# Performance work log

Hardware: AMD Instinct MI355X
Metric: run time of the kernel (lower is better)

Reference implementation:

```python
import jax, jax.numpy as jnp
import numpy as np

IN_F = 512
OUT_F = 256
ALPHA = 0.2  # LeakyReLU negative slope
NEG_INF = -9e15


def setup_inputs() -> dict:
    key = jax.random.key(0)
    k1, k2, k3, k4 = jax.random.split(key, 4)
    N = 8192
    inp = jax.random.normal(k1, (N, IN_F), dtype=jnp.float32)
    adj = jax.random.randint(k2, (N, N), 0, 2, dtype=jnp.int32)
    # xavier_normal with gain=1.414
    std_W = 1.414 * np.sqrt(2.0 / (IN_F + OUT_F))
    W = jax.random.normal(k3, (IN_F, OUT_F), dtype=jnp.float32) * std_W
    std_a = 1.414 * np.sqrt(2.0 / (2 * OUT_F + 1))
    a = jax.random.normal(k4, (2 * OUT_F, 1), dtype=jnp.float32) * std_a
    return {"input": inp, "adj": adj, "W": W, "a": a}


def reference(input, adj, W, a):
    h = input @ W                              # [N, F]
    attn_self = h @ a[:OUT_F]                  # [N, 1]
    attn_neigh = h @ a[OUT_F:]                 # [N, 1]
    dense = attn_self + attn_neigh.T           # [N, N] broadcast add
    dense = jnp.where(dense >= 0, dense, ALPHA * dense)  # leaky relu
    scores = jnp.where(adj > 0, dense, NEG_INF)
    attention = jax.nn.softmax(scores, axis=1)  # dropout p=0.0 -> identity
    h_prime = attention @ h                     # [N, F]
    return jax.nn.elu(h_prime)                  # concat=True branch
```

## Files before the change

kernel.cpp:

```cpp
#include <hip/hip_runtime.h>
#include <hip/hip_bf16.h>
#include <math.h>

#define DEVI static __device__ __forceinline__

using f32x4  = __attribute__((ext_vector_type(4))) float;
using f32x16 = __attribute__((ext_vector_type(16))) float;
using s16x8  = __attribute__((ext_vector_type(8))) short;
using bf16x8 = __attribute__((ext_vector_type(8))) __bf16;
using i32x4  = __attribute__((ext_vector_type(4))) int;
using u32x2  = __attribute__((ext_vector_type(2))) unsigned int;
using u32x4  = __attribute__((ext_vector_type(4))) unsigned int;

constexpr int N   = 8192;
constexpr int KIN = 512;
constexpr int F   = 256;

DEVI unsigned f2bf(float f) {
  unsigned u = __builtin_bit_cast(unsigned, f);
  return ((u + 0x7FFFu + ((u >> 16) & 1u)) >> 16) & 0xFFFFu;
}

DEVI float bfLO(unsigned u) { return __builtin_bit_cast(float, (u & 0xFFFFu) << 16); }
DEVI float bfHI(unsigned u) { return __builtin_bit_cast(float, u & 0xFFFF0000u); }

DEVI unsigned cvtpk(float lo, float hi) {
  unsigned r;
  asm("v_cvt_pk_bf16_f32 %0, %1, %2" : "=v"(r) : "v"(lo), "v"(hi));
  return r;
}

DEVI f32x16 mfma32(s16x8 a, s16x8 b, f32x16 c) {
  return __builtin_amdgcn_mfma_f32_32x32x16_bf16(
      __builtin_bit_cast(bf16x8, a), __builtin_bit_cast(bf16x8, b), c, 0, 0, 0);
}

DEVI void gload16(const void* g, void* lds_uniform) {
  __builtin_amdgcn_global_load_lds(
      (const __attribute__((address_space(1))) unsigned*)g,
      (__attribute__((address_space(3))) unsigned*)lds_uniform, 16, 0, 0);
}

__global__ __launch_bounds__(256) void k_cast(const float* __restrict__ src,
                                              unsigned short* __restrict__ dst,
                                              int n8) {
  int t = blockIdx.x * 256 + threadIdx.x;
  if (t >= n8) return;
  const f32x4* p = (const f32x4*)(src + (size_t)t * 8);
  f32x4 v0 = p[0], v1 = p[1];
  s16x8 o;
  o[0] = (short)f2bf(v0[0]); o[1] = (short)f2bf(v0[1]);
  o[2] = (short)f2bf(v0[2]); o[3] = (short)f2bf(v0[3]);
  o[4] = (short)f2bf(v1[0]); o[5] = (short)f2bf(v1[1]);
  o[6] = (short)f2bf(v1[2]); o[7] = (short)f2bf(v1[3]);
  *(s16x8*)(dst + (size_t)t * 8) = o;
}

__global__ __launch_bounds__(256) void k_prep_w(const float* __restrict__ W,
                                                unsigned short* __restrict__ Wt) {
  int t = blockIdx.x * 256 + threadIdx.x;
  int c = t >> 6, k0 = (t & 63) * 8;
  s16x8 o;
#pragma unroll
  for (int i = 0; i < 8; ++i) o[i] = (short)f2bf(W[(size_t)(k0 + i) * F + c]);
  *(s16x8*)(Wt + (size_t)c * KIN + k0) = o;
}

__global__ __launch_bounds__(512) void k_gemm1(const unsigned short* __restrict__ inpb,
                                               const unsigned short* __restrict__ Wt,
                                               const float* __restrict__ a_vec,
                                               unsigned short* __restrict__ Ht,
                                               float* __restrict__ E, float* __restrict__ E5,
                                               unsigned* __restrict__ FG) {
  __shared__ __align__(16) char lds[4096 + 32768 + 2048];
  char* ldsA = lds;
  char* ldsW = lds + 4096;
  float* red = (float*)(lds + 36864);
  int tid = threadIdx.x, w = tid >> 6, l = tid & 63;
  int r0 = blockIdx.x * 32;
  f32x16 acc;
#pragma unroll
  for (int i = 0; i < 16; ++i) acc[i] = 0.f;

  int lrow8 = l >> 3;
  int koffB = ((l & 7) ^ lrow8) * 8;
  int ra = l & 31, kb = (l >> 5) * 8;
  int colw = w * 32 + ra;

  for (int it = 0; it < 8; ++it) {
    int k0 = it * 64;
    __syncthreads();
    if (w < 4) {
      int row = 8 * w + lrow8;
      gload16(inpb + (size_t)(r0 + row) * KIN + k0 + koffB, ldsA + w * 1024);
    }
#pragma unroll
    for (int qi = 0; qi < 4; ++qi) {
      int q = 4 * w + qi;
      int c = 8 * q + lrow8;
      gload16(Wt + (size_t)c * KIN + k0 + koffB, ldsW + q * 1024);
    }
    __syncthreads();
    s16x8 av[4], bv[4];
#pragma unroll
    for (int kf = 0; kf < 4; ++kf) {
      int kk2 = (kf * 16 + kb) * 2;
      av[kf] = *(const s16x8*)(ldsA + ra * 128 + (kk2 ^ ((ra & 7) << 4)));
      bv[kf] = *(const s16x8*)(ldsW + colw * 128 + (kk2 ^ ((colw & 7) << 4)));
    }
#pragma unroll
    for (int kf = 0; kf < 4; ++kf) acc = mfma32(av[kf], bv[kf], acc);
  }

  float a1 = a_vec[colw], a2 = a_vec[256 + colw];
  int rquad = (l >> 5) * 4;
#pragma unroll
  for (int g = 0; g < 4; ++g) {
    int rowb = g * 8 + rquad;
    unsigned h0 = f2bf(acc[g * 4 + 0]), h1 = f2bf(acc[g * 4 + 1]);
    unsigned h2 = f2bf(acc[g * 4 + 2]), h3 = f2bf(acc[g * 4 + 3]);
    u32x2 pk;
    pk[0] = h0 | (h1 << 16);
    pk[1] = h2 | (h3 << 16);
    *(u32x2*)(Ht + (size_t)colw * N + r0 + rowb) = pk;
  }
#pragma unroll
  for (int g = 0; g < 16; ++g) {
    float vs = acc[g] * a1;
    float vn = acc[g] * a2;
#pragma unroll
    for (int m = 1; m <= 16; m <<= 1) {
      vs += __shfl_xor(vs, m, 64);
      vn += __shfl_xor(vn, m, 64);
    }
    if ((l & 31) == 0) {
      int row = (g & 3) + 8 * (g >> 2) + rquad;
      red[row * 8 + w] = vs;
      red[256 + row * 8 + w] = vn;
    }
  }
  __syncthreads();
  if (tid < 32) {
    float s = 0.f, n2 = 0.f;
#pragma unroll
    for (int i = 0; i < 8; ++i) { s += red[tid * 8 + i]; n2 += red[256 + tid * 8 + i]; }
    E[r0 + tid]  = expf(s);
    E5[r0 + tid] = expf(0.2f * s);
    FG[r0 + tid] = f2bf(expf(n2)) | (f2bf(expf(0.2f * n2)) << 16);
  }
}

__global__ __launch_bounds__(512, 4) void k_phase2(const int* __restrict__ adj,
                                                   const unsigned short* __restrict__ Ht,
                                                   const float* __restrict__ E,
                                                   const float* __restrict__ E5,
                                                   const unsigned* __restrict__ FG,
                                                   unsigned short* __restrict__ pacc,
                                                   float* __restrict__ ps) {
  __shared__ __align__(16) char lds[65536 + 8192];
  char* ldsH = lds;
  char* ldsP = lds + 65536;

  const int tid = threadIdx.x, w = tid >> 6, l = tid & 63;
  const int rb = blockIdx.x >> 2, ks = blockIdx.x & 3;
  const int r0 = rb * 64;
  const int jb = ks * 2048;

  const int r = tid >> 3, jc8 = (tid & 7) * 8;
  const float Er = E[r0 + r], E5r = E5[r0 + r];
  float s_part = 0.f;
  const int*      __restrict__ adjR = adj + (size_t)(r0 + r) * N + jb + jc8;
  const unsigned* __restrict__ fgR  = FG + jb + jc8;
  const int pw_byte = r * 128 + ((jc8 * 2) ^ ((r & 7) << 4));

  const int lrow8 = l >> 3;
  const int koffB = ((l & 7) ^ lrow8) * 8;
  const int rg = w >> 2, fg = w & 3;
  const int ra = rg * 32 + (l & 31);
  const int khb = (l >> 5) * 16;
  const int col0 = fg * 64 + (l & 31);
  const int col1 = col0 + 32;
  const int swz = (l & 7) << 4;

  f32x16 acc0, acc1;
#pragma unroll
  for (int i = 0; i < 16; ++i) { acc0[i] = 0.f; acc1[i] = 0.f; }

  i32x4 ad0 = *(const i32x4*)(adjR);
  i32x4 ad1 = *(const i32x4*)(adjR + 4);
  u32x4 fgc0 = *(const u32x4*)(fgR);
  u32x4 fgc1 = *(const u32x4*)(fgR + 4);
#pragma unroll
  for (int qi = 0; qi < 4; ++qi) {
    int q = 4 * w + qi;
    int c = 8 * q + lrow8;
    gload16(Ht + (size_t)c * N + jb + koffB, ldsH + q * 1024);
  }

  for (int it = 0; it < 32; ++it) {
    char* Hc = ldsH + (it & 1) * 32768;
    char* Hn = ldsH + ((it & 1) ^ 1) * 32768;
    const int itn = (it + 1) & 31;
    const int jn = itn * 64;

    i32x4 nad0 = *(const i32x4*)(adjR + jn);
    i32x4 nad1 = *(const i32x4*)(adjR + jn + 4);
    u32x4 nfg0 = *(const u32x4*)(fgR + jn);
    u32x4 nfg1 = *(const u32x4*)(fgR + jn + 4);

    {
      float p0 = (ad0[0] != 0) ? fmaxf(Er * bfLO(fgc0[0]), E5r * bfHI(fgc0[0])) : 0.f;
      float p1 = (ad0[1] != 0) ? fmaxf(Er * bfLO(fgc0[1]), E5r * bfHI(fgc0[1])) : 0.f;
      float p2 = (ad0[2] != 0) ? fmaxf(Er * bfLO(fgc0[2]), E5r * bfHI(fgc0[2])) : 0.f;
      float p3 = (ad0[3] != 0) ? fmaxf(Er * bfLO(fgc0[3]), E5r * bfHI(fgc0[3])) : 0.f;
      float p4 = (ad1[0] != 0) ? fmaxf(Er * bfLO(fgc1[0]), E5r * bfHI(fgc1[0])) : 0.f;
      float p5 = (ad1[1] != 0) ? fmaxf(Er * bfLO(fgc1[1]), E5r * bfHI(fgc1[1])) : 0.f;
      float p6 = (ad1[2] != 0) ? fmaxf(Er * bfLO(fgc1[2]), E5r * bfHI(fgc1[2])) : 0.f;
      float p7 = (ad1[3] != 0) ? fmaxf(Er * bfLO(fgc1[3]), E5r * bfHI(fgc1[3])) : 0.f;
      s_part += ((p0 + p1) + (p2 + p3)) + ((p4 + p5) + (p6 + p7));
      u32x4 pk;
      pk[0] = cvtpk(p0, p1); pk[1] = cvtpk(p2, p3);
      pk[2] = cvtpk(p4, p5); pk[3] = cvtpk(p6, p7);
      *(u32x4*)(ldsP + pw_byte) = pk;
    }

    asm volatile("s_waitcnt vmcnt(4) lgkmcnt(0)" ::: "memory");
    __builtin_amdgcn_s_barrier();

#pragma unroll
    for (int qi = 0; qi < 4; ++qi) {
      int q = 4 * w + qi;
      int c = 8 * q + lrow8;
      gload16(Ht + (size_t)c * N + jb + jn + koffB, Hn + q * 1024);
    }

#pragma unroll
    for (int kt = 0; kt < 4; ++kt) {
      int kk2 = kt * 32 + khb;
      s16x8 av = *(const s16x8*)(ldsP + ra * 128 + (kk2 ^ swz));
      s16x8 b0 = *(const s16x8*)(Hc + col0 * 128 + (kk2 ^ swz));
      s16x8 b1 = *(const s16x8*)(Hc + col1 * 128 + (kk2 ^ swz));
      acc0 = mfma32(av, b0, acc0);
      acc1 = mfma32(av, b1, acc1);
    }

    asm volatile("s_waitcnt lgkmcnt(0)" ::: "memory");
    __builtin_amdgcn_s_barrier();

    ad0 = nad0; ad1 = nad1; fgc0 = nfg0; fgc1 = nfg1;
  }

  float s = s_part;
#pragma unroll
  for (int m = 1; m <= 4; m <<= 1) s += __shfl_xor(s, m, 64);
  if ((tid & 7) == 0) ps[(size_t)ks * N + r0 + r] = s;

  unsigned short* po = pacc + (size_t)ks * N * F;
#pragma unroll
  for (int g = 0; g < 16; ++g) {
    int orow = rg * 32 + (g & 3) + 8 * (g >> 2) + 4 * (l >> 5);
    po[(size_t)(r0 + orow) * F + col0] = (unsigned short)f2bf(acc0[g]);
    po[(size_t)(r0 + orow) * F + col1] = (unsigned short)f2bf(acc1[g]);
  }
}

__global__ __launch_bounds__(256) void k_combine(const unsigned short* __restrict__ pacc,
                                                 const float* __restrict__ ps,
                                                 float* __restrict__ out) {
  int t = blockIdx.x * 256 + threadIdx.x;
  size_t idx = (size_t)t * 4;
  int row = (int)(idx >> 8);
  f32x4 sum;
#pragma unroll
  for (int i = 0; i < 4; ++i) sum[i] = 0.f;
#pragma unroll
  for (int k = 0; k < 4; ++k) {
    u32x2 q = *(const u32x2*)(pacc + (size_t)k * N * F + idx);
    sum[0] += bfLO(q[0]) * 1.f; sum[1] += bfHI(q[0]);
    sum[2] += bfLO(q[1]);       sum[3] += bfHI(q[1]);
  }
  float inv = 1.f / (ps[row] + ps[N + row] + ps[2 * N + row] + ps[3 * N + row]);
  f32x4 o;
#pragma unroll
  for (int i = 0; i < 4; ++i) {
    float v = sum[i] * inv;
    o[i] = v > 0.f ? v : expm1f(v);
  }
  *(f32x4*)(out + idx) = o;
}

extern "C" void kernel_launch(void* const* d_in, const int* in_sizes, int n_in,
                              void* d_out, int out_size, void* d_ws, size_t ws_size,
                              hipStream_t stream) {
  const float* input = (const float*)d_in[0];
  const int*   adj   = (const int*)d_in[1];
  const float* W     = (const float*)d_in[2];
  const float* a     = (const float*)d_in[3];
  float* out = (float*)d_out;
  char* ws = (char*)d_ws;

  unsigned short* pacc = (unsigned short*)(ws);
  unsigned short* inpb = (unsigned short*)(ws);
  unsigned short* Wt   = (unsigned short*)(ws + 8388608);
  unsigned short* Ht   = (unsigned short*)(ws + 16777216);
  float*    E  = (float*)(ws + 20971520);
  float*    E5 = (float*)(ws + 21004288);
  unsigned* FG = (unsigned*)(ws + 21037056);
  float*    ps = (float*)(ws + 21069824);

  hipLaunchKernelGGL(k_cast,   dim3(2048), dim3(256), 0, stream, input, inpb, 524288);
  hipLaunchKernelGGL(k_prep_w, dim3(64),   dim3(256), 0, stream, W, Wt);
  hipLaunchKernelGGL(k_gemm1,  dim3(256),  dim3(512), 0, stream, inpb, Wt, a, Ht, E, E5, FG);
  hipLaunchKernelGGL(k_phase2, dim3(512),  dim3(512), 0, stream, adj, Ht, E, E5, FG, pacc, ps);
  hipLaunchKernelGGL(k_combine,dim3(2048), dim3(256), 0, stream, pacc, ps, out);
}
```

Baseline: 117.3 us.

## Double row tile in attention kernel and double-buffer P to drop a barrier

Phase-2 blocks now cover 128 rows instead of 64, so each staged H tile in LDS feeds twice as many rows. Each wave keeps four MFMA accumulators over 128 output columns. The P tile is now double-buffered in LDS, which removes the second barrier per iteration. In exchange, the grid halves to 256 blocks, so there is less parallelism on a large-CU GPU. LDS use and register pressure also rise, and the occupancy hint in the launch bounds is removed.

```diff
diff --git a/kernel.cpp b/kernel.cpp
--- a/kernel.cpp
+++ b/kernel.cpp
@@ -150,46 +150,52 @@
   }
 }
 
-__global__ __launch_bounds__(512, 4) void k_phase2(const int* __restrict__ adj,
-                                                   const unsigned short* __restrict__ Ht,
-                                                   const float* __restrict__ E,
-                                                   const float* __restrict__ E5,
-                                                   const unsigned* __restrict__ FG,
-                                                   unsigned short* __restrict__ pacc,
-                                                   float* __restrict__ ps) {
-  __shared__ __align__(16) char lds[65536 + 8192];
+__global__ __launch_bounds__(512) void k_phase2(const int* __restrict__ adj,
+                                                const unsigned short* __restrict__ Ht,
+                                                const float* __restrict__ E,
+                                                const float* __restrict__ E5,
+                                                const unsigned* __restrict__ FG,
+                                                unsigned short* __restrict__ pacc,
+                                                float* __restrict__ ps) {
+  __shared__ __align__(16) char lds[65536 + 32768];
   char* ldsH = lds;
   char* ldsP = lds + 65536;
 
   const int tid = threadIdx.x, w = tid >> 6, l = tid & 63;
   const int rb = blockIdx.x >> 2, ks = blockIdx.x & 3;
-  const int r0 = rb * 64;
+  const int r0 = rb * 128;
   const int jb = ks * 2048;
 
-  const int r = tid >> 3, jc8 = (tid & 7) * 8;
+  const int r = tid >> 2, j16 = (tid & 3) * 16;
   const float Er = E[r0 + r], E5r = E5[r0 + r];
   float s_part = 0.f;
-  const int*      __restrict__ adjR = adj + (size_t)(r0 + r) * N + jb + jc8;
-  const unsigned* __restrict__ fgR  = FG + jb + jc8;
-  const int pw_byte = r * 128 + ((jc8 * 2) ^ ((r & 7) << 4));
+  const int*      __restrict__ adjR = adj + (size_t)(r0 + r) * N + jb + j16;
+  const unsigned* __restrict__ fgR  = FG + jb + j16;
+  const int pw0 = r * 128 + ((j16 * 2) ^ ((r & 7) << 4));
+  const int pw1 = pw0 ^ 16;
 
   const int lrow8 = l >> 3;
   const int koffB = ((l & 7) ^ lrow8) * 8;
-  const int rg = w >> 2, fg = w & 3;
+
+  const int rg = w >> 1, fgi = w & 1;
   const int ra = rg * 32 + (l & 31);
   const int khb = (l >> 5) * 16;
-  const int col0 = fg * 64 + (l & 31);
-  const int col1 = col0 + 32;
-  const int swz = (l & 7) << 4;
-
-  f32x16 acc0, acc1;
-#pragma unroll
-  for (int i = 0; i < 16; ++i) { acc0[i] = 0.f; acc1[i] = 0.f; }
+  const int colb = fgi * 128 + (l & 31);
+  const int swzA = (ra & 7) << 4;
+  const int swzB = (l & 7) << 4;
+
+  f32x16 acc0, acc1, acc2, acc3;
+#pragma unroll
+  for (int i = 0; i < 16; ++i) { acc0[i] = 0.f; acc1[i] = 0.f; acc2[i] = 0.f; acc3[i] = 0.f; }
 
   i32x4 ad0 = *(const i32x4*)(adjR);
   i32x4 ad1 = *(const i32x4*)(adjR + 4);
-  u32x4 fgc0 = *(const u32x4*)(fgR);
-  u32x4 fgc1 = *(const u32x4*)(fgR + 4);
+  i32x4 ad2 = *(const i32x4*)(adjR + 8);
+  i32x4 ad3 = *(const i32x4*)(adjR + 12);
+  u32x4 fc0 = *(const u32x4*)(fgR);
+  u32x4 fc1 = *(const u32x4*)(fgR + 4);
+  u32x4 fc2 = *(const u32x4*)(fgR + 8);
+  u32x4 fc3 = *(const u32x4*)(fgR + 12);
 #pragma unroll
   for (int qi = 0; qi < 4; ++qi) {
     int q = 4 * w + qi;
@@ -200,31 +206,48 @@
   for (int it = 0; it < 32; ++it) {
     char* Hc = ldsH + (it & 1) * 32768;
     char* Hn = ldsH + ((it & 1) ^ 1) * 32768;
-    const int itn = (it + 1) & 31;
-    const int jn = itn * 64;
+    char* Pc = ldsP + (it & 1) * 16384;
+    const int jn = ((it + 1) & 31) * 64;
 
     i32x4 nad0 = *(const i32x4*)(adjR + jn);
     i32x4 nad1 = *(const i32x4*)(adjR + jn + 4);
-    u32x4 nfg0 = *(const u32x4*)(fgR + jn);
-    u32x4 nfg1 = *(const u32x4*)(fgR + jn + 4);
+    i32x4 nad2 = *(const i32x4*)(adjR + jn + 8);
+    i32x4 nad3 = *(const i32x4*)(adjR + jn + 12);
+    u32x4 nfc0 = *(const u32x4*)(fgR + jn);
+    u32x4 nfc1 = *(const u32x4*)(fgR + jn + 4);
+    u32x4 nfc2 = *(const u32x4*)(fgR + jn + 8);
+    u32x4 nfc3 = *(const u32x4*)(fgR + jn + 12);
 
     {
-      float p0 = (ad0[0] != 0) ? fmaxf(Er * bfLO(fgc0[0]), E5r * bfHI(fgc0[0])) : 0.f;
-      float p1 = (ad0[1] != 0) ? fmaxf(Er * bfLO(fgc0[1]), E5r * bfHI(fgc0[1])) : 0.f;
-      float p2 = (ad0[2] != 0) ? fmaxf(Er * bfLO(fgc0[2]), E5r * bfHI(fgc0[2])) : 0.f;
-      float p3 = (ad0[3] != 0) ? fmaxf(Er * bfLO(fgc0[3]), E5r * bfHI(fgc0[3])) : 0.f;
-      float p4 = (ad1[0] != 0) ? fmaxf(Er * bfLO(fgc1[0]), E5r * bfHI(fgc1[0])) : 0.f;
-      float p5 = (ad1[1] != 0) ? fmaxf(Er * bfLO(fgc1[1]), E5r * bfHI(fgc1[1])) : 0.f;
-      float p6 = (ad1[2] != 0) ? fmaxf(Er * bfLO(fgc1[2]), E5r * bfHI(fgc1[2])) : 0.f;
-      float p7 = (ad1[3] != 0) ? fmaxf(Er * bfLO(fgc1[3]), E5r * bfHI(fgc1[3])) : 0.f;
+      float p0, p1, p2, p3, p4, p5, p6, p7;
+      u32x4 pkA, pkB;
+      p0 = (ad0[0] != 0) ? fmaxf(Er * bfLO(fc0[0]), E5r * bfHI(fc0[0])) : 0.f;
+      p1 = (ad0[1] != 0) ? fmaxf(Er * bfLO(fc0[1]), E5r * bfHI(fc0[1])) : 0.f;
+      p2 = (ad0[2] != 0) ? fmaxf(Er * bfLO(fc0[2]), E5r * bfHI(fc0[2])) : 0.f;
+      p3 = (ad0[3] != 0) ? fmaxf(Er * bfLO(fc0[3]), E5r * bfHI(fc0[3])) : 0.f;
+      p4 = (ad1[0] != 0) ? fmaxf(Er * bfLO(fc1[0]), E5r * bfHI(fc1[0])) : 0.f;
+      p5 = (ad1[1] != 0) ? fmaxf(Er * bfLO(fc1[1]), E5r * bfHI(fc1[1])) : 0.f;
+      p6 = (ad1[2] != 0) ? fmaxf(Er * bfLO(fc1[2]), E5r * bfHI(fc1[2])) : 0.f;
+      p7 = (ad1[3] != 0) ? fmaxf(Er * bfLO(fc1[3]), E5r * bfHI(fc1[3])) : 0.f;
       s_part += ((p0 + p1) + (p2 + p3)) + ((p4 + p5) + (p6 + p7));
-      u32x4 pk;
-      pk[0] = cvtpk(p0, p1); pk[1] = cvtpk(p2, p3);
-      pk[2] = cvtpk(p4, p5); pk[3] = cvtpk(p6, p7);
-      *(u32x4*)(ldsP + pw_byte) = pk;
-    }
-
-    asm volatile("s_waitcnt vmcnt(4) lgkmcnt(0)" ::: "memory");
+      pkA[0] = cvtpk(p0, p1); pkA[1] = cvtpk(p2, p3);
+      pkA[2] = cvtpk(p4, p5); pkA[3] = cvtpk(p6, p7);
+      p0 = (ad2[0] != 0) ? fmaxf(Er * bfLO(fc2[0]), E5r * bfHI(fc2[0])) : 0.f;
+      p1 = (ad2[1] != 0) ? fmaxf(Er * bfLO(fc2[1]), E5r * bfHI(fc2[1])) : 0.f;
+      p2 = (ad2[2] != 0) ? fmaxf(Er * bfLO(fc2[2]), E5r * bfHI(fc2[2])) : 0.f;
+      p3 = (ad2[3] != 0) ? fmaxf(Er * bfLO(fc2[3]), E5r * bfHI(fc2[3])) : 0.f;
+      p4 = (ad3[0] != 0) ? fmaxf(Er * bfLO(fc3[0]), E5r * bfHI(fc3[0])) : 0.f;
+      p5 = (ad3[1] != 0) ? fmaxf(Er * bfLO(fc3[1]), E5r * bfHI(fc3[1])) : 0.f;
+      p6 = (ad3[2] != 0) ? fmaxf(Er * bfLO(fc3[2]), E5r * bfHI(fc3[2])) : 0.f;
+      p7 = (ad3[3] != 0) ? fmaxf(Er * bfLO(fc3[3]), E5r * bfHI(fc3[3])) : 0.f;
+      s_part += ((p0 + p1) + (p2 + p3)) + ((p4 + p5) + (p6 + p7));
+      pkB[0] = cvtpk(p0, p1); pkB[1] = cvtpk(p2, p3);
+      pkB[2] = cvtpk(p4, p5); pkB[3] = cvtpk(p6, p7);
+      *(u32x4*)(Pc + pw0) = pkA;
+      *(u32x4*)(Pc + pw1) = pkB;
+    }
+
+    asm volatile("s_waitcnt vmcnt(8) lgkmcnt(0)" ::: "memory");
     __builtin_amdgcn_s_barrier();
 
 #pragma unroll
@@ -237,30 +260,35 @@
 #pragma unroll
     for (int kt = 0; kt < 4; ++kt) {
       int kk2 = kt * 32 + khb;
-      s16x8 av = *(const s16x8*)(ldsP + ra * 128 + (kk2 ^ swz));
-      s16x8 b0 = *(const s16x8*)(Hc + col0 * 128 + (kk2 ^ swz));
-      s16x8 b1 = *(const s16x8*)(Hc + col1 * 128 + (kk2 ^ swz));
+      s16x8 av = *(const s16x8*)(Pc + ra * 128 + (kk2 ^ swzA));
+      s16x8 b0 = *(const s16x8*)(Hc + (colb) * 128 + (kk2 ^ swzB));
+      s16x8 b1 = *(const s16x8*)(Hc + (colb + 32) * 128 + (kk2 ^ swzB));
+      s16x8 b2 = *(const s16x8*)(Hc + (colb + 64) * 128 + (kk2 ^ swzB));
+      s16x8 b3 = *(const s16x8*)(Hc + (colb + 96) * 128 + (kk2 ^ swzB));
       acc0 = mfma32(av, b0, acc0);
       acc1 = mfma32(av, b1, acc1);
-    }
-
-    asm volatile("s_waitcnt lgkmcnt(0)" ::: "memory");
-    __builtin_amdgcn_s_barrier();
-
-    ad0 = nad0; ad1 = nad1; fgc0 = nfg0; fgc1 = nfg1;
+      acc2 = mfma32(av, b2, acc2);
+      acc3 = mfma32(av, b3, acc3);
+    }
+
+    ad0 = nad0; ad1 = nad1; ad2 = nad2; ad3 = nad3;
+    fc0 = nfc0; fc1 = nfc1; fc2 = nfc2; fc3 = nfc3;
   }
 
   float s = s_part;
 #pragma unroll
-  for (int m = 1; m <= 4; m <<= 1) s += __shfl_xor(s, m, 64);
-  if ((tid & 7) == 0) ps[(size_t)ks * N + r0 + r] = s;
+  for (int m = 1; m <= 2; m <<= 1) s += __shfl_xor(s, m, 64);
+  if ((tid & 3) == 0) ps[(size_t)ks * N + r0 + r] = s;
 
   unsigned short* po = pacc + (size_t)ks * N * F;
 #pragma unroll
   for (int g = 0; g < 16; ++g) {
     int orow = rg * 32 + (g & 3) + 8 * (g >> 2) + 4 * (l >> 5);
-    po[(size_t)(r0 + orow) * F + col0] = (unsigned short)f2bf(acc0[g]);
-    po[(size_t)(r0 + orow) * F + col1] = (unsigned short)f2bf(acc1[g]);
+    unsigned short* pr = po + (size_t)(r0 + orow) * F + colb;
+    pr[0]  = (unsigned short)f2bf(acc0[g]);
+    pr[32] = (unsigned short)f2bf(acc1[g]);
+    pr[64] = (unsigned short)f2bf(acc2[g]);
+    pr[96] = (unsigned short)f2bf(acc3[g]);
   }
 }
 
@@ -276,8 +304,8 @@
 #pragma unroll
   for (int k = 0; k < 4; ++k) {
     u32x2 q = *(const u32x2*)(pacc + (size_t)k * N * F + idx);
-    sum[0] += bfLO(q[0]) * 1.f; sum[1] += bfHI(q[0]);
-    sum[2] += bfLO(q[1]);       sum[3] += bfHI(q[1]);
+    sum[0] += bfLO(q[0]); sum[1] += bfHI(q[0]);
+    sum[2] += bfLO(q[1]); sum[3] += bfHI(q[1]);
   }
   float inv = 1.f / (ps[row] + ps[N + row] + ps[2 * N + row] + ps[3 * N + row]);
   f32x4 o;
@@ -311,6 +339,6 @@
   hipLaunchKernelGGL(k_cast,   dim3(2048), dim3(256), 0, stream, input, inpb, 524288);
   hipLaunchKernelGGL(k_prep_w, dim3(64),   dim3(256), 0, stream, W, Wt);
   hipLaunchKernelGGL(k_gemm1,  dim3(256),  dim3(512), 0, stream, inpb, Wt, a, Ht, E, E5, FG);
-  hipLaunchKernelGGL(k_phase2, dim3(512),  dim3(512), 0, stream, adj, Ht, E, E5, FG, pacc, ps);
+  hipLaunchKernelGGL(k_phase2, dim3(256),  dim3(512), 0, stream, adj, Ht, E, E5, FG, pacc, ps);
   hipLaunchKernelGGL(k_combine,dim3(2048), dim3(256), 0, stream, pacc, ps, out);
 }
```

Result: slower. 128.2 us (+9.3%).

## Split MFMA work along K across warp halves with LDS reduction of accumulators

Applied to the files above, without the earlier changes.

Reassigns the eight warps so each computes a 32x128 output tile over half of the 64-wide K step, which raises A-fragment reuse per LDS read (one A read feeds four MFMAs instead of two). The two K-halves are then summed through LDS before one half writes bf16 partials. It also moves the next-iteration adj/FG global loads to after the P computation to cut live registers. The cost is double the accumulator registers per warp and an extra LDS reduction plus barriers in the epilogue.

```diff
diff --git a/kernel.cpp b/kernel.cpp
--- a/kernel.cpp
+++ b/kernel.cpp
@@ -175,48 +175,44 @@
 
   const int lrow8 = l >> 3;
   const int koffB = ((l & 7) ^ lrow8) * 8;
-  const int rg = w >> 2, fg = w & 3;
+
+  const int kh = w >> 2, fgp = (w >> 1) & 1, rg = w & 1;
   const int ra = rg * 32 + (l & 31);
   const int khb = (l >> 5) * 16;
-  const int col0 = fg * 64 + (l & 31);
-  const int col1 = col0 + 32;
-  const int swz = (l & 7) << 4;
-
-  f32x16 acc0, acc1;
-#pragma unroll
-  for (int i = 0; i < 16; ++i) { acc0[i] = 0.f; acc1[i] = 0.f; }
-
-  i32x4 ad0 = *(const i32x4*)(adjR);
-  i32x4 ad1 = *(const i32x4*)(adjR + 4);
-  u32x4 fgc0 = *(const u32x4*)(fgR);
-  u32x4 fgc1 = *(const u32x4*)(fgR + 4);
+  const int colb = fgp * 128 + (l & 31);
+  const int swzA = (ra & 7) << 4;
+  const int swzB = (l & 7) << 4;
+  const int kt0 = kh * 2;
+
+  f32x16 acc0, acc1, acc2, acc3;
+#pragma unroll
+  for (int i = 0; i < 16; ++i) { acc0[i] = 0.f; acc1[i] = 0.f; acc2[i] = 0.f; acc3[i] = 0.f; }
+
 #pragma unroll
   for (int qi = 0; qi < 4; ++qi) {
     int q = 4 * w + qi;
     int c = 8 * q + lrow8;
     gload16(Ht + (size_t)c * N + jb + koffB, ldsH + q * 1024);
   }
+  i32x4 ad0 = *(const i32x4*)(adjR);
+  i32x4 ad1 = *(const i32x4*)(adjR + 4);
+  u32x4 fc0 = *(const u32x4*)(fgR);
+  u32x4 fc1 = *(const u32x4*)(fgR + 4);
 
   for (int it = 0; it < 32; ++it) {
     char* Hc = ldsH + (it & 1) * 32768;
     char* Hn = ldsH + ((it & 1) ^ 1) * 32768;
-    const int itn = (it + 1) & 31;
-    const int jn = itn * 64;
-
-    i32x4 nad0 = *(const i32x4*)(adjR + jn);
-    i32x4 nad1 = *(const i32x4*)(adjR + jn + 4);
-    u32x4 nfg0 = *(const u32x4*)(fgR + jn);
-    u32x4 nfg1 = *(const u32x4*)(fgR + jn + 4);
+    const int jn = ((it + 1) & 31) * 64;
 
     {
-      float p0 = (ad0[0] != 0) ? fmaxf(Er * bfLO(fgc0[0]), E5r * bfHI(fgc0[0])) : 0.f;
-      float p1 = (ad0[1] != 0) ? fmaxf(Er * bfLO(fgc0[1]), E5r * bfHI(fgc0[1])) : 0.f;
-      float p2 = (ad0[2] != 0) ? fmaxf(Er * bfLO(fgc0[2]), E5r * bfHI(fgc0[2])) : 0.f;
-      float p3 = (ad0[3] != 0) ? fmaxf(Er * bfLO(fgc0[3]), E5r * bfHI(fgc0[3])) : 0.f;
-      float p4 = (ad1[0] != 0) ? fmaxf(Er * bfLO(fgc1[0]), E5r * bfHI(fgc1[0])) : 0.f;
-      float p5 = (ad1[1] != 0) ? fmaxf(Er * bfLO(fgc1[1]), E5r * bfHI(fgc1[1])) : 0.f;
-      float p6 = (ad1[2] != 0) ? fmaxf(Er * bfLO(fgc1[2]), E5r * bfHI(fgc1[2])) : 0.f;
-      float p7 = (ad1[3] != 0) ? fmaxf(Er * bfLO(fgc1[3]), E5r * bfHI(fgc1[3])) : 0.f;
+      float p0 = (ad0[0] != 0) ? fmaxf(Er * bfLO(fc0[0]), E5r * bfHI(fc0[0])) : 0.f;
+      float p1 = (ad0[1] != 0) ? fmaxf(Er * bfLO(fc0[1]), E5r * bfHI(fc0[1])) : 0.f;
+      float p2 = (ad0[2] != 0) ? fmaxf(Er * bfLO(fc0[2]), E5r * bfHI(fc0[2])) : 0.f;
+      float p3 = (ad0[3] != 0) ? fmaxf(Er * bfLO(fc0[3]), E5r * bfHI(fc0[3])) : 0.f;
+      float p4 = (ad1[0] != 0) ? fmaxf(Er * bfLO(fc1[0]), E5r * bfHI(fc1[0])) : 0.f;
+      float p5 = (ad1[1] != 0) ? fmaxf(Er * bfLO(fc1[1]), E5r * bfHI(fc1[1])) : 0.f;
+      float p6 = (ad1[2] != 0) ? fmaxf(Er * bfLO(fc1[2]), E5r * bfHI(fc1[2])) : 0.f;
+      float p7 = (ad1[3] != 0) ? fmaxf(Er * bfLO(fc1[3]), E5r * bfHI(fc1[3])) : 0.f;
       s_part += ((p0 + p1) + (p2 + p3)) + ((p4 + p5) + (p6 + p7));
       u32x4 pk;
       pk[0] = cvtpk(p0, p1); pk[1] = cvtpk(p2, p3);
@@ -224,6 +220,11 @@
       *(u32x4*)(ldsP + pw_byte) = pk;
     }
 
+    ad0 = *(const i32x4*)(adjR + jn);
+    ad1 = *(const i32x4*)(adjR + jn + 4);
+    fc0 = *(const u32x4*)(fgR + jn);
+    fc1 = *(const u32x4*)(fgR + jn + 4);
+
     asm volatile("s_waitcnt vmcnt(4) lgkmcnt(0)" ::: "memory");
     __builtin_amdgcn_s_barrier();
 
@@ -235,19 +236,21 @@
     }
 
 #pragma unroll
-    for (int kt = 0; kt < 4; ++kt) {
-      int kk2 = kt * 32 + khb;
-      s16x8 av = *(const s16x8*)(ldsP + ra * 128 + (kk2 ^ swz));
-      s16x8 b0 = *(const s16x8*)(Hc + col0 * 128 + (kk2 ^ swz));
-      s16x8 b1 = *(const s16x8*)(Hc + col1 * 128 + (kk2 ^ swz));
+    for (int t2 = 0; t2 < 2; ++t2) {
+      int kk2 = (kt0 + t2) * 32 + khb;
+      s16x8 av = *(const s16x8*)(ldsP + ra * 128 + (kk2 ^ swzA));
+      s16x8 b0 = *(const s16x8*)(Hc + (colb     ) * 128 + (kk2 ^ swzB));
+      s16x8 b1 = *(const s16x8*)(Hc + (colb + 32) * 128 + (kk2 ^ swzB));
+      s16x8 b2 = *(const s16x8*)(Hc + (colb + 64) * 128 + (kk2 ^ swzB));
+      s16x8 b3 = *(const s16x8*)(Hc + (colb + 96) * 128 + (kk2 ^ swzB));
       acc0 = mfma32(av, b0, acc0);
       acc1 = mfma32(av, b1, acc1);
+      acc2 = mfma32(av, b2, acc2);
+      acc3 = mfma32(av, b3, acc3);
     }
 
     asm volatile("s_waitcnt lgkmcnt(0)" ::: "memory");
     __builtin_amdgcn_s_barrier();
-
-    ad0 = nad0; ad1 = nad1; fgc0 = nfg0; fgc1 = nfg1;
   }
 
   float s = s_part;
@@ -255,12 +258,46 @@
   for (int m = 1; m <= 4; m <<= 1) s += __shfl_xor(s, m, 64);
   if ((tid & 7) == 0) ps[(size_t)ks * N + r0 + r] = s;
 
-  unsigned short* po = pacc + (size_t)ks * N * F;
-#pragma unroll
-  for (int g = 0; g < 16; ++g) {
-    int orow = rg * 32 + (g & 3) + 8 * (g >> 2) + 4 * (l >> 5);
-    po[(size_t)(r0 + orow) * F + col0] = (unsigned short)f2bf(acc0[g]);
-    po[(size_t)(r0 + orow) * F + col1] = (unsigned short)f2bf(acc1[g]);
+  __syncthreads();
+  float* red = (float*)ldsH;
+  const int rbase = (fgp * 2 + rg) * 4096;
+  if (kh == 1) {
+#pragma unroll
+    for (int cg = 0; cg < 4; ++cg) {
+      const f32x16* a = (cg == 0) ? &acc0 : (cg == 1) ? &acc1 : (cg == 2) ? &acc2 : &acc3;
+#pragma unroll
+      for (int q = 0; q < 4; ++q) {
+        f32x4 v;
+#pragma unroll
+        for (int i = 0; i < 4; ++i) v[i] = (*a)[q * 4 + i];
+        int boff = (cg * 64 + q * 16) ^ ((l & 7) << 4);
+        *(f32x4*)((char*)&red[rbase + l * 64] + boff) = v;
+      }
+    }
+  }
+  __syncthreads();
+  if (kh == 0) {
+#pragma unroll
+    for (int cg = 0; cg < 4; ++cg) {
+      f32x16* a = (cg == 0) ? &acc0 : (cg == 1) ? &acc1 : (cg == 2) ? &acc2 : &acc3;
+#pragma unroll
+      for (int q = 0; q < 4; ++q) {
+        int boff = (cg * 64 + q * 16) ^ ((l & 7) << 4);
+        f32x4 v = *(const f32x4*)((const char*)&red[rbase + l * 64] + boff);
+#pragma unroll
+        for (int i = 0; i < 4; ++i) (*a)[q * 4 + i] += v[i];
+      }
+    }
+    unsigned short* po = pacc + (size_t)ks * N * F;
+#pragma unroll
+    for (int g = 0; g < 16; ++g) {
+      int orow = rg * 32 + (g & 3) + 8 * (g >> 2) + 4 * (l >> 5);
+      unsigned short* pr = po + (size_t)(r0 + orow) * F + colb;
+      pr[0]  = (unsigned short)f2bf(acc0[g]);
+      pr[32] = (unsigned short)f2bf(acc1[g]);
+      pr[64] = (unsigned short)f2bf(acc2[g]);
+      pr[96] = (unsigned short)f2bf(acc3[g]);
+    }
   }
 }
 
@@ -276,8 +313,8 @@
 #pragma unroll
   for (int k = 0; k < 4; ++k) {
     u32x2 q = *(const u32x2*)(pacc + (size_t)k * N * F + idx);
-    sum[0] += bfLO(q[0]) * 1.f; sum[1] += bfHI(q[0]);
-    sum[2] += bfLO(q[1]);       sum[3] += bfHI(q[1]);
+    sum[0] += bfLO(q[0]); sum[1] += bfHI(q[0]);
+    sum[2] += bfLO(q[1]); sum[3] += bfHI(q[1]);
   }
   float inv = 1.f / (ps[row] + ps[N + row] + ps[2 * N + row] + ps[3 * N + row]);
   f32x4 o;
```

Measured after the change: 114.3 us. 2.5% less time.
